# Kernel optimization log

Measured on AMD Instinct MI355X. Metric: run time of the kernel, lower is better.

The kernel has to match this reference:

```python
import jax, jax.numpy as jnp
import numpy as np

B, S, D, H = 2, 2048, 1024, 16
DK = D // H

def setup_inputs() -> dict:
    key = jax.random.key(0)
    ks = jax.random.split(key, 7)
    q = jax.random.normal(ks[0], (B, S, D), dtype=jnp.float32)
    k = jax.random.normal(ks[1], (B, S, D), dtype=jnp.float32)
    v = jax.random.normal(ks[2], (B, S, D), dtype=jnp.float32)
    # causal mask, broadcastable to [B, H, S, S]
    mask = jnp.tril(jnp.ones((S, S), dtype=jnp.int32))[None, None, :, :]
    sc = 1.0 / np.sqrt(D)
    Wq = jax.random.normal(ks[3], (D, D), dtype=jnp.float32) * sc
    Wk = jax.random.normal(ks[4], (D, D), dtype=jnp.float32) * sc
    Wv = jax.random.normal(ks[5], (D, D), dtype=jnp.float32) * sc
    Wo = jax.random.normal(ks[6], (D, D), dtype=jnp.float32) * sc
    return {"q": q, "k": k, "v": v, "mask": mask, "Wq": Wq, "Wk": Wk, "Wv": Wv, "Wo": Wo}

def reference(q, k, v, mask, Wq, Wk, Wv, Wo):
    # Linear projections (nn.Linear stores W as [out,in]; y = x @ W.T; here W is [D,D])
    query = jnp.einsum('bsd,ed->bse', q, Wq).reshape(B, S, H, DK).transpose(0, 2, 1, 3)
    key_  = jnp.einsum('bsd,ed->bse', k, Wk).reshape(B, S, H, DK).transpose(0, 2, 1, 3)
    value = jnp.einsum('bsd,ed->bse', v, Wv).reshape(B, S, H, DK).transpose(0, 2, 1, 3)
    # scaled dot-product attention, full [B,H,S,S] scores (as in the original)
    scaled_qk = jnp.einsum('bhqd,bhkd->bhqk', query, key_) / np.sqrt(DK)
    scaled_qk = jnp.where(mask == 0, jnp.float32(-1e9), scaled_qk)
    scores = jax.nn.softmax(scaled_qk, axis=-1)
    # dropout_rate = 0.0 -> identity
    attn = jnp.einsum('bhqk,bhkd->bhqd', scores, value)
    x = attn.transpose(0, 2, 1, 3).reshape(B, S, D)
    return jnp.einsum('bsd,ed->bse', x, Wo)
```

## Files before the change

### kernel.cpp

```cpp
#include <hip/hip_runtime.h>

constexpr int Bv  = 2;
constexpr int Sv  = 2048;
constexpr int Dv  = 1024;
constexpr int Hv  = 16;
constexpr int DKv = 64;
constexpr int NTOK = Bv * Sv;

#define QSCALE 0.18033688011112042f

typedef __attribute__((ext_vector_type(8))) short bf16x8;
typedef __attribute__((ext_vector_type(4))) float f32x4;

__device__ __forceinline__ ushort f2bf(float f) {
  unsigned int u = __float_as_uint(f);
  unsigned int r = (u + 0x7fffu + ((u >> 16) & 1u)) >> 16;
  return (ushort)r;
}

__device__ __forceinline__ float fast_exp2(float x) {
#if __has_builtin(__builtin_amdgcn_exp2f)
  return __builtin_amdgcn_exp2f(x);
#else
  return exp2f(x);
#endif
}

__device__ __forceinline__ int swz(int byte_linear, int row) {
  return byte_linear ^ ((row & 7) << 4);
}

__device__ __forceinline__ void cast_octet(const float* __restrict__ src,
                                           ushort* __restrict__ dst, int o) {
  const float4 f0 = *reinterpret_cast<const float4*>(src + (size_t)o * 8);
  const float4 f1 = *reinterpret_cast<const float4*>(src + (size_t)o * 8 + 4);
  uint4 u;
  u.x = (unsigned int)f2bf(f0.x) | ((unsigned int)f2bf(f0.y) << 16);
  u.y = (unsigned int)f2bf(f0.z) | ((unsigned int)f2bf(f0.w) << 16);
  u.z = (unsigned int)f2bf(f1.x) | ((unsigned int)f2bf(f1.y) << 16);
  u.w = (unsigned int)f2bf(f1.z) | ((unsigned int)f2bf(f1.w) << 16);
  *reinterpret_cast<uint4*>(dst + (size_t)o * 8) = u;
}

__device__ __forceinline__ void split_octet(const float* __restrict__ src,
                                            ushort* __restrict__ dst, int o) {
  const float4 f0 = *reinterpret_cast<const float4*>(src + (size_t)o * 8);
  const float4 f1 = *reinterpret_cast<const float4*>(src + (size_t)o * 8 + 4);
  float xs[8] = {f0.x, f0.y, f0.z, f0.w, f1.x, f1.y, f1.z, f1.w};
  unsigned int hp[4], lp[4];
#pragma unroll
  for (int j = 0; j < 4; ++j) {
    const unsigned int u0 = __float_as_uint(xs[2 * j]);
    const unsigned int u1 = __float_as_uint(xs[2 * j + 1]);
    const unsigned int h0 = u0 & 0xffff0000u;
    const unsigned int h1 = u1 & 0xffff0000u;
    hp[j] = (h0 >> 16) | h1;
    const float r0 = xs[2 * j] - __uint_as_float(h0);
    const float r1 = xs[2 * j + 1] - __uint_as_float(h1);
    lp[j] = (__float_as_uint(r0) >> 16) | (__float_as_uint(r1) & 0xffff0000u);
  }
  uint4* d = reinterpret_cast<uint4*>(dst + (size_t)o * 16);
  d[0] = make_uint4(hp[0], hp[1], hp[2], hp[3]);
  d[1] = make_uint4(lp[0], lp[1], lp[2], lp[3]);
}

__global__ __launch_bounds__(256)
void cast_split(const float* __restrict__ q, const float* __restrict__ k,
                const float* __restrict__ v, const float* __restrict__ Wq,
                const float* __restrict__ Wk, const float* __restrict__ Wv,
                const float* __restrict__ Wo,
                ushort* __restrict__ qB, ushort* __restrict__ kB,
                ushort* __restrict__ vB, ushort* __restrict__ WqB,
                ushort* __restrict__ WkB, ushort* __restrict__ WvB,
                ushort* __restrict__ WoS) {
  const int o = blockIdx.x * 256 + threadIdx.x;
  constexpr int NA = NTOK * Dv / 8;
  constexpr int NW = Dv * Dv / 8;
  switch (blockIdx.y) {
    case 0: if (o < NA) cast_octet(q, qB, o); break;
    case 1: if (o < NA) cast_octet(k, kB, o); break;
    case 2: if (o < NA) cast_octet(v, vB, o); break;
    case 3: if (o < NW) cast_octet(Wq, WqB, o); break;
    case 4: if (o < NW) cast_octet(Wk, WkB, o); break;
    case 5: if (o < NW) cast_octet(Wv, WvB, o); break;
    default: if (o < NW) split_octet(Wo, WoS, o); break;
  }
}

__global__ __launch_bounds__(256)
void split1(const float* __restrict__ src, ushort* __restrict__ dst) {
  const int o = blockIdx.x * 256 + threadIdx.x;
  if (o < NTOK * Dv / 8) split_octet(src, dst, o);
}

__global__ __launch_bounds__(256, 2)
void gemm_qkv_bf16(const ushort* __restrict__ qB, const ushort* __restrict__ kB,
                   const ushort* __restrict__ vB,
                   const ushort* __restrict__ WqB, const ushort* __restrict__ WkB,
                   const ushort* __restrict__ WvB,
                   ushort* __restrict__ Qw, ushort* __restrict__ Kw,
                   ushort* __restrict__ Vw) {
  const int hid = (int)blockIdx.z * 256 + (int)blockIdx.y * 8 + (int)blockIdx.x;
  const int id  = (hid & 7) * 96 + (hid >> 3);
  const int bn = id & 7;
  const int bm = (id >> 3) & 31;
  const int bz = id >> 8;

  const ushort* Ag;
  const ushort* Wg;
  ushort* Y;
  float scale = 1.0f;
  if (bz == 0)      { Ag = qB; Wg = WqB; Y = Qw; scale = QSCALE; }
  else if (bz == 1) { Ag = kB; Wg = WkB; Y = Kw; }
  else              { Ag = vB; Wg = WvB; Y = Vw; }

  __shared__ __align__(16) ushort AT[128 * 128];
  __shared__ __align__(16) ushort WT[128 * 128];

  const int tid  = threadIdx.x;
  const int lane = tid & 63;
  const int wid  = tid >> 6;
  const int wr = wid >> 1, wc = wid & 1;
  const int c = lane & 15, g = lane >> 4;

  f32x4 acc[4][4];
#pragma unroll
  for (int m = 0; m < 4; ++m)
#pragma unroll
    for (int n = 0; n < 4; ++n) acc[m][n] = (f32x4){0.f, 0.f, 0.f, 0.f};

  const int srow  = tid >> 4;
  const int sslot = tid & 15;
  const size_t aBase = (size_t)(bm * 128 + srow) * 1024 + sslot * 8;
  const size_t wBase = (size_t)(bn * 128 + srow) * 1024 + sslot * 8;
  const int sb = srow * 256 + ((sslot * 16) ^ ((srow & 7) << 4));

  for (int kt = 0; kt < 8; ++kt) {
    __syncthreads();
#pragma unroll
    for (int it = 0; it < 8; ++it)
      *reinterpret_cast<uint4*>((char*)AT + it * 4096 + sb) =
          *reinterpret_cast<const uint4*>(Ag + aBase + (size_t)it * 16384 + kt * 128);
#pragma unroll
    for (int it = 0; it < 8; ++it)
      *reinterpret_cast<uint4*>((char*)WT + it * 4096 + sb) =
          *reinterpret_cast<const uint4*>(Wg + wBase + (size_t)it * 16384 + kt * 128);
    __syncthreads();

#pragma unroll
    for (int kk = 0; kk < 4; ++kk) {
      const int ob = kk * 64 + 16 * g;
      bf16x8 bh[4];
#pragma unroll
      for (int n = 0; n < 4; ++n) {
        const int row = wc * 64 + n * 16 + c;
        bh[n] = *reinterpret_cast<const bf16x8*>((const char*)WT + swz(row * 256 + ob, row));
      }
#pragma unroll
      for (int m = 0; m < 4; ++m) {
        const int row = wr * 64 + m * 16 + c;
        const bf16x8 ah = *reinterpret_cast<const bf16x8*>((const char*)AT + swz(row * 256 + ob, row));
#pragma unroll
        for (int n = 0; n < 4; ++n)
          acc[m][n] = __builtin_amdgcn_mfma_f32_16x16x32_bf16(ah, bh[n], acc[m][n], 0, 0, 0);
      }
    }
  }

#pragma unroll
  for (int m = 0; m < 4; ++m)
#pragma unroll
    for (int n = 0; n < 4; ++n)
#pragma unroll
      for (int r = 0; r < 4; ++r) {
        const int tok = bm * 128 + wr * 64 + m * 16 + 4 * g + r;
        const int e   = bn * 128 + wc * 64 + n * 16 + c;
        const int bb = tok >> 11, ss = tok & (Sv - 1);
        const int hh = e >> 6, dk = e & (DKv - 1);
        Y[(((size_t)bb * Hv + hh) * Sv + ss) * DKv + dk] = f2bf(acc[m][n][r] * scale);
      }
}

__global__ __launch_bounds__(256, 2)
void gemm_out_mfma(const ushort* __restrict__ Ag, const ushort* __restrict__ Wg,
                   float* __restrict__ out) {
  const int hid = (int)blockIdx.y * 8 + (int)blockIdx.x;
  const int id  = (hid & 7) * 32 + (hid >> 3);
  const int bn = id & 7;
  const int bm = id >> 3;

  __shared__ __align__(16) ushort AT[128 * 128];
  __shared__ __align__(16) ushort WT[128 * 128];

  const int tid  = threadIdx.x;
  const int lane = tid & 63;
  const int wid  = tid >> 6;
  const int wr = wid >> 1, wc = wid & 1;
  const int c = lane & 15, g = lane >> 4;

  f32x4 acc[4][4];
#pragma unroll
  for (int m = 0; m < 4; ++m)
#pragma unroll
    for (int n = 0; n < 4; ++n) acc[m][n] = (f32x4){0.f, 0.f, 0.f, 0.f};

  const int srow  = tid >> 4;
  const int sslot = tid & 15;
  const size_t aBase = (size_t)(bm * 128 + srow) * 2048 + sslot * 8;
  const size_t wBase = (size_t)(bn * 128 + srow) * 2048 + sslot * 8;
  const int sb = srow * 256 + ((sslot * 16) ^ ((srow & 7) << 4));

  for (int kt = 0; kt < 16; ++kt) {
    __syncthreads();
#pragma unroll
    for (int it = 0; it < 8; ++it)
      *reinterpret_cast<uint4*>((char*)AT + it * 4096 + sb) =
          *reinterpret_cast<const uint4*>(Ag + aBase + (size_t)it * 32768 + kt * 128);
#pragma unroll
    for (int it = 0; it < 8; ++it)
      *reinterpret_cast<uint4*>((char*)WT + it * 4096 + sb) =
          *reinterpret_cast<const uint4*>(Wg + wBase + (size_t)it * 32768 + kt * 128);
    __syncthreads();

#pragma unroll
    for (int kk = 0; kk < 2; ++kk) {
      const int ob = (kk * 4 + g) * 32;
      bf16x8 bh[4], bl[4];
#pragma unroll
      for (int n = 0; n < 4; ++n) {
        const int row = wc * 64 + n * 16 + c;
        const char* p = (const char*)WT;
        bh[n] = *reinterpret_cast<const bf16x8*>(p + swz(row * 256 + ob, row));
        bl[n] = *reinterpret_cast<const bf16x8*>(p + swz(row * 256 + ob + 16, row));
      }
#pragma unroll
      for (int m = 0; m < 4; ++m) {
        const int row = wr * 64 + m * 16 + c;
        const char* p = (const char*)AT;
        const bf16x8 ah = *reinterpret_cast<const bf16x8*>(p + swz(row * 256 + ob, row));
        const bf16x8 al = *reinterpret_cast<const bf16x8*>(p + swz(row * 256 + ob + 16, row));
#pragma unroll
        for (int n = 0; n < 4; ++n) {
          acc[m][n] = __builtin_amdgcn_mfma_f32_16x16x32_bf16(ah, bh[n], acc[m][n], 0, 0, 0);
          acc[m][n] = __builtin_amdgcn_mfma_f32_16x16x32_bf16(al, bh[n], acc[m][n], 0, 0, 0);
          acc[m][n] = __builtin_amdgcn_mfma_f32_16x16x32_bf16(ah, bl[n], acc[m][n], 0, 0, 0);
        }
      }
    }
  }

#pragma unroll
  for (int m = 0; m < 4; ++m)
#pragma unroll
    for (int n = 0; n < 4; ++n)
#pragma unroll
      for (int r = 0; r < 4; ++r) {
        const int tok = bm * 128 + wr * 64 + m * 16 + 4 * g + r;
        const int e   = bn * 128 + wc * 64 + n * 16 + c;
        out[(size_t)tok * Dv + e] = acc[m][n][r];
      }
}

__global__ __launch_bounds__(256)
void attn_fwd_mfma(const ushort* __restrict__ Q, const ushort* __restrict__ K,
                   const ushort* __restrict__ V, float* __restrict__ X) {
  const int tid  = threadIdx.x;
  const int lane = tid & 63;
  const int w    = tid >> 6;
  const int c    = lane & 15;
  const int g    = lane >> 4;
  const int qt = (int)gridDim.x - 1 - (int)blockIdx.x;
  const int bh = blockIdx.y;
  const int b = bh >> 4, h = bh & (Hv - 1);
  const int qtk = 2 * qt + 1;

  const ushort* Qb = Q + (size_t)bh * Sv * DKv;
  const ushort* Kb = K + (size_t)bh * Sv * DKv;
  const ushort* Vb = V + (size_t)bh * Sv * DKv;

  __shared__ __align__(16) char lds[49152];

#pragma unroll
  for (int l = 0; l < 2; ++l) {
    const int r  = l * 64 + (tid >> 2);
    const int c0 = (tid & 3) << 4;
    const ushort* src = Qb + (size_t)(qt * 128 + r) * DKv + c0;
    uint4 v0 = *reinterpret_cast<const uint4*>(src);
    uint4 v1 = *reinterpret_cast<const uint4*>(src + 8);
    *reinterpret_cast<uint4*>(lds + swz(r * 128 + 2 * c0, r))      = v0;
    *reinterpret_cast<uint4*>(lds + swz(r * 128 + 2 * c0 + 16, r)) = v1;
  }
  __syncthreads();

  bf16x8 qf0[2], qf1[2];
#pragma unroll
  for (int m = 0; m < 2; ++m) {
    const int qr = w * 32 + m * 16 + c;
    qf0[m] = *reinterpret_cast<const bf16x8*>(lds + swz(qr * 128 + 16 * g, qr));
    qf1[m] = *reinterpret_cast<const bf16x8*>(lds + swz(qr * 128 + 64 + 16 * g, qr));
  }

  const int kr_s  = tid >> 2;
  const int kc_s  = (tid & 3) << 4;
  const int vi_s  = tid & 31;
  const int vc_s  = (tid >> 5) << 3;

  uint4 kA, kB, vA, vB;
  {
    const ushort* ks = Kb + (size_t)kr_s * DKv + kc_s;
    kA = *reinterpret_cast<const uint4*>(ks);
    kB = *reinterpret_cast<const uint4*>(ks + 8);
    const ushort* vs = Vb + (size_t)(2 * vi_s) * DKv + vc_s;
    vA = *reinterpret_cast<const uint4*>(vs);
    vB = *reinterpret_cast<const uint4*>(vs + DKv);
  }
  __syncthreads();

  {
    char* kd = lds;
    *reinterpret_cast<uint4*>(kd + swz(kr_s * 128 + 2 * kc_s, kr_s))      = kA;
    *reinterpret_cast<uint4*>(kd + swz(kr_s * 128 + 2 * kc_s + 16, kr_s)) = kB;
    char* vd = lds + 16384;
    unsigned int ee[4] = {vA.x, vA.y, vA.z, vA.w};
    unsigned int oo[4] = {vB.x, vB.y, vB.z, vB.w};
#pragma unroll
    for (int p = 0; p < 4; ++p) {
      unsigned int lo = (ee[p] & 0xffffu) | (oo[p] << 16);
      unsigned int hi = (ee[p] >> 16) | (oo[p] & 0xffff0000u);
      const int d0 = vc_s + 2 * p;
      *reinterpret_cast<unsigned int*>(vd + swz(d0 * 128 + 4 * vi_s, d0))           = lo;
      *reinterpret_cast<unsigned int*>(vd + swz((d0 + 1) * 128 + 4 * vi_s, d0 + 1)) = hi;
    }
  }
  __syncthreads();

  f32x4 accO[2][4];
#pragma unroll
  for (int m = 0; m < 2; ++m)
#pragma unroll
    for (int ds = 0; ds < 4; ++ds) accO[m][ds] = (f32x4){0.f, 0.f, 0.f, 0.f};
  float mS[2] = {-3.0e38f, -3.0e38f};
  float lS[2] = {0.f, 0.f};

  for (int kv = 0; kv <= qtk; ++kv) {
    const int cur = kv & 1;

    if (kv < qtk) {
      const ushort* ks = Kb + (size_t)((kv + 1) * 64 + kr_s) * DKv + kc_s;
      kA = *reinterpret_cast<const uint4*>(ks);
      kB = *reinterpret_cast<const uint4*>(ks + 8);
      const ushort* vs = Vb + (size_t)((kv + 1) * 64 + 2 * vi_s) * DKv + vc_s;
      vA = *reinterpret_cast<const uint4*>(vs);
      vB = *reinterpret_cast<const uint4*>(vs + DKv);
    }

    const char* kbase = lds + cur * 8192;
    const char* vbase = lds + 16384 + cur * 8192;
    char* pbase = lds + 32768 + w * 4096;

    f32x4 s[2][4];
#pragma unroll
    for (int kt = 0; kt < 4; ++kt) {
      const int kr = kt * 16 + c;
      bf16x8 kf0 = *reinterpret_cast<const bf16x8*>(kbase + swz(kr * 128 + 16 * g, kr));
      bf16x8 kf1 = *reinterpret_cast<const bf16x8*>(kbase + swz(kr * 128 + 64 + 16 * g, kr));
#pragma unroll
      for (int m = 0; m < 2; ++m) {
        f32x4 z = (f32x4){0.f, 0.f, 0.f, 0.f};
        z = __builtin_amdgcn_mfma_f32_16x16x32_bf16(kf0, qf0[m], z, 0, 0, 0);
        s[m][kt] = __builtin_amdgcn_mfma_f32_16x16x32_bf16(kf1, qf1[m], z, 0, 0, 0);
      }
    }

    if (kv >= 2 * qt) {
#pragma unroll
      for (int m = 0; m < 2; ++m) {
        const int ql = qt * 128 + w * 32 + m * 16 + c;
#pragma unroll
        for (int kt = 0; kt < 4; ++kt)
#pragma unroll
          for (int rr = 0; rr < 4; ++rr) {
            const int kl = kv * 64 + kt * 16 + 4 * g + rr;
            if (kl > ql) s[m][kt][rr] = -3.0e38f;
          }
      }
    }

    float corrM[2];
#pragma unroll
    for (int m = 0; m < 2; ++m) {
      float tm = -3.0e38f;
#pragma unroll
      for (int kt = 0; kt < 4; ++kt)
#pragma unroll
        for (int rr = 0; rr < 4; ++rr) tm = fmaxf(tm, s[m][kt][rr]);
      tm = fmaxf(tm, __shfl_xor(tm, 16));
      tm = fmaxf(tm, __shfl_xor(tm, 32));
      const float mnew = fmaxf(mS[m], tm);
      corrM[m] = fast_exp2(mS[m] - mnew);
      mS[m] = mnew;

      float psum = 0.f;
#pragma unroll
      for (int kt = 0; kt < 4; ++kt)
#pragma unroll
        for (int rr = 0; rr < 4; ++rr) {
          const float p = fast_exp2(s[m][kt][rr] - mnew);
          s[m][kt][rr] = p;
          psum += p;
        }
      psum += __shfl_xor(psum, 16);
      psum += __shfl_xor(psum, 32);
      lS[m] = lS[m] * corrM[m] + psum;

      const int pr = m * 16 + c;
#pragma unroll
      for (int kt = 0; kt < 4; ++kt) {
        unsigned int lo = (unsigned int)f2bf(s[m][kt][0]) | ((unsigned int)f2bf(s[m][kt][1]) << 16);
        unsigned int hi = (unsigned int)f2bf(s[m][kt][2]) | ((unsigned int)f2bf(s[m][kt][3]) << 16);
        const int k0 = kt * 16 + 4 * g;
        *reinterpret_cast<unsigned int*>(pbase + swz(pr * 128 + 2 * k0, pr))     = lo;
        *reinterpret_cast<unsigned int*>(pbase + swz(pr * 128 + 2 * k0 + 4, pr)) = hi;
      }

      float corr4[4];
#pragma unroll
      for (int rr = 0; rr < 4; ++rr)
        corr4[rr] = __int_as_float(__builtin_amdgcn_ds_bpermute(
            (4 * g + rr) << 2, __float_as_int(corrM[m])));
#pragma unroll
      for (int ds = 0; ds < 4; ++ds)
#pragma unroll
        for (int rr = 0; rr < 4; ++rr) accO[m][ds][rr] *= corr4[rr];
    }

#pragma unroll
    for (int ks = 0; ks < 2; ++ks) {
      bf16x8 vf[4];
#pragma unroll
      for (int ds = 0; ds < 4; ++ds) {
        const int dk = ds * 16 + c;
        vf[ds] = *reinterpret_cast<const bf16x8*>(vbase + swz(dk * 128 + ks * 64 + 16 * g, dk));
      }
#pragma unroll
      for (int m = 0; m < 2; ++m) {
        const int pr = m * 16 + c;
        bf16x8 pf = *reinterpret_cast<const bf16x8*>(pbase + swz(pr * 128 + ks * 64 + 16 * g, pr));
#pragma unroll
        for (int ds = 0; ds < 4; ++ds)
          accO[m][ds] = __builtin_amdgcn_mfma_f32_16x16x32_bf16(pf, vf[ds], accO[m][ds], 0, 0, 0);
      }
    }

    if (kv < qtk) {
      char* kd = lds + (cur ^ 1) * 8192;
      *reinterpret_cast<uint4*>(kd + swz(kr_s * 128 + 2 * kc_s, kr_s))      = kA;
      *reinterpret_cast<uint4*>(kd + swz(kr_s * 128 + 2 * kc_s + 16, kr_s)) = kB;
      char* vd = lds + 16384 + (cur ^ 1) * 8192;
      unsigned int ee[4] = {vA.x, vA.y, vA.z, vA.w};
      unsigned int oo[4] = {vB.x, vB.y, vB.z, vB.w};
#pragma unroll
      for (int p = 0; p < 4; ++p) {
        unsigned int lo = (ee[p] & 0xffffu) | (oo[p] << 16);
        unsigned int hi = (ee[p] >> 16) | (oo[p] & 0xffff0000u);
        const int d0 = vc_s + 2 * p;
        *reinterpret_cast<unsigned int*>(vd + swz(d0 * 128 + 4 * vi_s, d0))           = lo;
        *reinterpret_cast<unsigned int*>(vd + swz((d0 + 1) * 128 + 4 * vi_s, d0 + 1)) = hi;
      }
    }
    __syncthreads();
  }

#pragma unroll
  for (int m = 0; m < 2; ++m) {
    const float inv = 1.0f / lS[m];
    float inv4[4];
#pragma unroll
    for (int rr = 0; rr < 4; ++rr)
      inv4[rr] = __int_as_float(__builtin_amdgcn_ds_bpermute(
          (4 * g + rr) << 2, __float_as_int(inv)));
    const int q0 = qt * 128 + w * 32 + m * 16;
#pragma unroll
    for (int ds = 0; ds < 4; ++ds)
#pragma unroll
      for (int rr = 0; rr < 4; ++rr) {
        const int srow = q0 + 4 * g + rr;
        X[((size_t)(b * Sv + srow)) * Dv + h * DKv + ds * 16 + c] = accO[m][ds][rr] * inv4[rr];
      }
  }
}

extern "C" void kernel_launch(void* const* d_in, const int* in_sizes, int n_in,
                              void* d_out, int out_size, void* d_ws, size_t ws_size,
                              hipStream_t stream) {
  const float* q  = (const float*)d_in[0];
  const float* k  = (const float*)d_in[1];
  const float* v  = (const float*)d_in[2];
  const float* Wq = (const float*)d_in[4];
  const float* Wk = (const float*)d_in[5];
  const float* Wv = (const float*)d_in[6];
  const float* Wo = (const float*)d_in[7];
  float* out = (float*)d_out;

  constexpr size_t SEG   = (size_t)NTOK * Dv;
  constexpr size_t ACT_S = SEG * 2;
  constexpr size_t X_S   = SEG * 4;
  constexpr size_t WB_S  = (size_t)Dv * Dv * 2;
  constexpr size_t SPW_S = (size_t)Dv * Dv * 4;

  char* ws = (char*)d_ws;
  ushort* Qw  = (ushort*)(ws);
  ushort* Kw  = (ushort*)(ws + ACT_S);
  ushort* Vw  = (ushort*)(ws + 2 * ACT_S);
  float*  Xw  = (float*) (ws + 3 * ACT_S);
  ushort* qB  = (ushort*)(ws + 3 * ACT_S + X_S);
  ushort* kB  = (ushort*)(ws + 3 * ACT_S + X_S + ACT_S);
  ushort* vB  = (ushort*)(ws + 3 * ACT_S + X_S + 2 * ACT_S);
  ushort* WqB = (ushort*)(ws + 3 * ACT_S + X_S + 3 * ACT_S);
  ushort* WkB = (ushort*)(ws + 3 * ACT_S + X_S + 3 * ACT_S + WB_S);
  ushort* WvB = (ushort*)(ws + 3 * ACT_S + X_S + 3 * ACT_S + 2 * WB_S);
  ushort* WoS = (ushort*)(ws + 3 * ACT_S + X_S + 3 * ACT_S + 3 * WB_S);
  ushort* XS  = (ushort*)(ws + 3 * ACT_S + X_S + 3 * ACT_S + 3 * WB_S + SPW_S);

  const dim3 blk(256);
  cast_split<<<dim3(NTOK * Dv / 8 / 256, 7), blk, 0, stream>>>(
      q, k, v, Wq, Wk, Wv, Wo, qB, kB, vB, WqB, WkB, WvB, WoS);
  gemm_qkv_bf16<<<dim3(8, 32, 3), blk, 0, stream>>>(
      qB, kB, vB, WqB, WkB, WvB, Qw, Kw, Vw);
  attn_fwd_mfma<<<dim3(Sv / 128, Bv * Hv), blk, 0, stream>>>(Qw, Kw, Vw, Xw);
  split1<<<dim3(NTOK * Dv / 8 / 256), blk, 0, stream>>>(Xw, XS);
  gemm_out_mfma<<<dim3(8, 32), blk, 0, stream>>>(XS, WoS, out);
}
```

Measured before the change: 275.5 us.

## Fuse bf16 hi/lo split into attention epilogue and balance causal work per block

```diff
diff --git a/kernel.cpp b/kernel.cpp
--- a/kernel.cpp
+++ b/kernel.cpp
@@ -87,12 +87,6 @@
   }
 }
 
-__global__ __launch_bounds__(256)
-void split1(const float* __restrict__ src, ushort* __restrict__ dst) {
-  const int o = blockIdx.x * 256 + threadIdx.x;
-  if (o < NTOK * Dv / 8) split_octet(src, dst, o);
-}
-
 __global__ __launch_bounds__(256, 2)
 void gemm_qkv_bf16(const ushort* __restrict__ qB, const ushort* __restrict__ kB,
                    const ushort* __restrict__ vB,
@@ -261,202 +255,65 @@
       }
 }
 
-__global__ __launch_bounds__(256)
+__global__ __launch_bounds__(512)
 void attn_fwd_mfma(const ushort* __restrict__ Q, const ushort* __restrict__ K,
-                   const ushort* __restrict__ V, float* __restrict__ X) {
+                   const ushort* __restrict__ V, ushort* __restrict__ XS) {
   const int tid  = threadIdx.x;
   const int lane = tid & 63;
   const int w    = tid >> 6;
   const int c    = lane & 15;
   const int g    = lane >> 4;
-  const int qt = (int)gridDim.x - 1 - (int)blockIdx.x;
-  const int bh = blockIdx.y;
-  const int b = bh >> 4, h = bh & (Hv - 1);
-  const int qtk = 2 * qt + 1;
-
-  const ushort* Qb = Q + (size_t)bh * Sv * DKv;
-  const ushort* Kb = K + (size_t)bh * Sv * DKv;
-  const ushort* Vb = V + (size_t)bh * Sv * DKv;
 
   __shared__ __align__(16) char lds[49152];
 
-#pragma unroll
-  for (int l = 0; l < 2; ++l) {
-    const int r  = l * 64 + (tid >> 2);
-    const int c0 = (tid & 3) << 4;
-    const ushort* src = Qb + (size_t)(qt * 128 + r) * DKv + c0;
-    uint4 v0 = *reinterpret_cast<const uint4*>(src);
-    uint4 v1 = *reinterpret_cast<const uint4*>(src + 8);
-    *reinterpret_cast<uint4*>(lds + swz(r * 128 + 2 * c0, r))      = v0;
-    *reinterpret_cast<uint4*>(lds + swz(r * 128 + 2 * c0 + 16, r)) = v1;
-  }
-  __syncthreads();
-
-  bf16x8 qf0[2], qf1[2];
-#pragma unroll
-  for (int m = 0; m < 2; ++m) {
-    const int qr = w * 32 + m * 16 + c;
-    qf0[m] = *reinterpret_cast<const bf16x8*>(lds + swz(qr * 128 + 16 * g, qr));
-    qf1[m] = *reinterpret_cast<const bf16x8*>(lds + swz(qr * 128 + 64 + 16 * g, qr));
-  }
-
-  const int kr_s  = tid >> 2;
-  const int kc_s  = (tid & 3) << 4;
-  const int vi_s  = tid & 31;
-  const int vc_s  = (tid >> 5) << 3;
-
-  uint4 kA, kB, vA, vB;
-  {
-    const ushort* ks = Kb + (size_t)kr_s * DKv + kc_s;
-    kA = *reinterpret_cast<const uint4*>(ks);
-    kB = *reinterpret_cast<const uint4*>(ks + 8);
-    const ushort* vs = Vb + (size_t)(2 * vi_s) * DKv + vc_s;
-    vA = *reinterpret_cast<const uint4*>(vs);
-    vB = *reinterpret_cast<const uint4*>(vs + DKv);
-  }
-  __syncthreads();
-
-  {
-    char* kd = lds;
-    *reinterpret_cast<uint4*>(kd + swz(kr_s * 128 + 2 * kc_s, kr_s))      = kA;
-    *reinterpret_cast<uint4*>(kd + swz(kr_s * 128 + 2 * kc_s + 16, kr_s)) = kB;
-    char* vd = lds + 16384;
-    unsigned int ee[4] = {vA.x, vA.y, vA.z, vA.w};
-    unsigned int oo[4] = {vB.x, vB.y, vB.z, vB.w};
-#pragma unroll
-    for (int p = 0; p < 4; ++p) {
-      unsigned int lo = (ee[p] & 0xffffu) | (oo[p] << 16);
-      unsigned int hi = (ee[p] >> 16) | (oo[p] & 0xffff0000u);
-      const int d0 = vc_s + 2 * p;
-      *reinterpret_cast<unsigned int*>(vd + swz(d0 * 128 + 4 * vi_s, d0))           = lo;
-      *reinterpret_cast<unsigned int*>(vd + swz((d0 + 1) * 128 + 4 * vi_s, d0 + 1)) = hi;
-    }
-  }
-  __syncthreads();
-
-  f32x4 accO[2][4];
-#pragma unroll
-  for (int m = 0; m < 2; ++m)
-#pragma unroll
-    for (int ds = 0; ds < 4; ++ds) accO[m][ds] = (f32x4){0.f, 0.f, 0.f, 0.f};
-  float mS[2] = {-3.0e38f, -3.0e38f};
-  float lS[2] = {0.f, 0.f};
-
-  for (int kv = 0; kv <= qtk; ++kv) {
-    const int cur = kv & 1;
-
-    if (kv < qtk) {
-      const ushort* ks = Kb + (size_t)((kv + 1) * 64 + kr_s) * DKv + kc_s;
-      kA = *reinterpret_cast<const uint4*>(ks);
-      kB = *reinterpret_cast<const uint4*>(ks + 8);
-      const ushort* vs = Vb + (size_t)((kv + 1) * 64 + 2 * vi_s) * DKv + vc_s;
+  const int kr_s = tid >> 3;
+  const int kcb  = (tid & 7) << 4;
+  const bool vwork = (tid < 256);
+  const int vi_s = tid & 31;
+  const int vc_s = ((tid >> 5) & 7) << 3;
+
+#pragma unroll 1
+  for (int item = 0; item < 2; ++item) {
+    const int idx = (item == 0) ? (int)blockIdx.x : 511 - (int)blockIdx.x;
+    const int qt = idx >> 5;
+    const int bh = idx & 31;
+    const int b = bh >> 4, h = bh & (Hv - 1);
+    const int qtk = 2 * qt + 1;
+
+    const ushort* Qb = Q + (size_t)bh * Sv * DKv;
+    const ushort* Kb = K + (size_t)bh * Sv * DKv;
+    const ushort* Vb = V + (size_t)bh * Sv * DKv;
+
+    {
+      const int r  = tid >> 2;
+      const int c0 = (tid & 3) << 4;
+      const ushort* src = Qb + (size_t)(qt * 128 + r) * DKv + c0;
+      uint4 v0 = *reinterpret_cast<const uint4*>(src);
+      uint4 v1 = *reinterpret_cast<const uint4*>(src + 8);
+      *reinterpret_cast<uint4*>(lds + swz(r * 128 + 2 * c0, r))      = v0;
+      *reinterpret_cast<uint4*>(lds + swz(r * 128 + 2 * c0 + 16, r)) = v1;
+    }
+    __syncthreads();
+
+    bf16x8 qf0, qf1;
+    {
+      const int qr = w * 16 + c;
+      qf0 = *reinterpret_cast<const bf16x8*>(lds + swz(qr * 128 + 16 * g, qr));
+      qf1 = *reinterpret_cast<const bf16x8*>(lds + swz(qr * 128 + 64 + 16 * g, qr));
+    }
+
+    uint4 kA, vA, vB;
+    kA = *reinterpret_cast<const uint4*>((const char*)Kb + (size_t)kr_s * 128 + kcb);
+    if (vwork) {
+      const ushort* vs = Vb + (size_t)(2 * vi_s) * DKv + vc_s;
       vA = *reinterpret_cast<const uint4*>(vs);
       vB = *reinterpret_cast<const uint4*>(vs + DKv);
     }
-
-    const char* kbase = lds + cur * 8192;
-    const char* vbase = lds + 16384 + cur * 8192;
-    char* pbase = lds + 32768 + w * 4096;
-
-    f32x4 s[2][4];
-#pragma unroll
-    for (int kt = 0; kt < 4; ++kt) {
-      const int kr = kt * 16 + c;
-      bf16x8 kf0 = *reinterpret_cast<const bf16x8*>(kbase + swz(kr * 128 + 16 * g, kr));
-      bf16x8 kf1 = *reinterpret_cast<const bf16x8*>(kbase + swz(kr * 128 + 64 + 16 * g, kr));
-#pragma unroll
-      for (int m = 0; m < 2; ++m) {
-        f32x4 z = (f32x4){0.f, 0.f, 0.f, 0.f};
-        z = __builtin_amdgcn_mfma_f32_16x16x32_bf16(kf0, qf0[m], z, 0, 0, 0);
-        s[m][kt] = __builtin_amdgcn_mfma_f32_16x16x32_bf16(kf1, qf1[m], z, 0, 0, 0);
-      }
-    }
-
-    if (kv >= 2 * qt) {
-#pragma unroll
-      for (int m = 0; m < 2; ++m) {
-        const int ql = qt * 128 + w * 32 + m * 16 + c;
-#pragma unroll
-        for (int kt = 0; kt < 4; ++kt)
-#pragma unroll
-          for (int rr = 0; rr < 4; ++rr) {
-            const int kl = kv * 64 + kt * 16 + 4 * g + rr;
-            if (kl > ql) s[m][kt][rr] = -3.0e38f;
-          }
-      }
-    }
-
-    float corrM[2];
-#pragma unroll
-    for (int m = 0; m < 2; ++m) {
-      float tm = -3.0e38f;
-#pragma unroll
-      for (int kt = 0; kt < 4; ++kt)
-#pragma unroll
-        for (int rr = 0; rr < 4; ++rr) tm = fmaxf(tm, s[m][kt][rr]);
-      tm = fmaxf(tm, __shfl_xor(tm, 16));
-      tm = fmaxf(tm, __shfl_xor(tm, 32));
-      const float mnew = fmaxf(mS[m], tm);
-      corrM[m] = fast_exp2(mS[m] - mnew);
-      mS[m] = mnew;
-
-      float psum = 0.f;
-#pragma unroll
-      for (int kt = 0; kt < 4; ++kt)
-#pragma unroll
-        for (int rr = 0; rr < 4; ++rr) {
-          const float p = fast_exp2(s[m][kt][rr] - mnew);
-          s[m][kt][rr] = p;
-          psum += p;
-        }
-      psum += __shfl_xor(psum, 16);
-      psum += __shfl_xor(psum, 32);
-      lS[m] = lS[m] * corrM[m] + psum;
-
-      const int pr = m * 16 + c;
-#pragma unroll
-      for (int kt = 0; kt < 4; ++kt) {
-        unsigned int lo = (unsigned int)f2bf(s[m][kt][0]) | ((unsigned int)f2bf(s[m][kt][1]) << 16);
-        unsigned int hi = (unsigned int)f2bf(s[m][kt][2]) | ((unsigned int)f2bf(s[m][kt][3]) << 16);
-        const int k0 = kt * 16 + 4 * g;
-        *reinterpret_cast<unsigned int*>(pbase + swz(pr * 128 + 2 * k0, pr))     = lo;
-        *reinterpret_cast<unsigned int*>(pbase + swz(pr * 128 + 2 * k0 + 4, pr)) = hi;
-      }
-
-      float corr4[4];
-#pragma unroll
-      for (int rr = 0; rr < 4; ++rr)
-        corr4[rr] = __int_as_float(__builtin_amdgcn_ds_bpermute(
-            (4 * g + rr) << 2, __float_as_int(corrM[m])));
-#pragma unroll
-      for (int ds = 0; ds < 4; ++ds)
-#pragma unroll
-        for (int rr = 0; rr < 4; ++rr) accO[m][ds][rr] *= corr4[rr];
-    }
-
-#pragma unroll
-    for (int ks = 0; ks < 2; ++ks) {
-      bf16x8 vf[4];
-#pragma unroll
-      for (int ds = 0; ds < 4; ++ds) {
-        const int dk = ds * 16 + c;
-        vf[ds] = *reinterpret_cast<const bf16x8*>(vbase + swz(dk * 128 + ks * 64 + 16 * g, dk));
-      }
-#pragma unroll
-      for (int m = 0; m < 2; ++m) {
-        const int pr = m * 16 + c;
-        bf16x8 pf = *reinterpret_cast<const bf16x8*>(pbase + swz(pr * 128 + ks * 64 + 16 * g, pr));
-#pragma unroll
-        for (int ds = 0; ds < 4; ++ds)
-          accO[m][ds] = __builtin_amdgcn_mfma_f32_16x16x32_bf16(pf, vf[ds], accO[m][ds], 0, 0, 0);
-      }
-    }
-
-    if (kv < qtk) {
-      char* kd = lds + (cur ^ 1) * 8192;
-      *reinterpret_cast<uint4*>(kd + swz(kr_s * 128 + 2 * kc_s, kr_s))      = kA;
-      *reinterpret_cast<uint4*>(kd + swz(kr_s * 128 + 2 * kc_s + 16, kr_s)) = kB;
-      char* vd = lds + 16384 + (cur ^ 1) * 8192;
+    __syncthreads();
+
+    *reinterpret_cast<uint4*>(lds + swz(kr_s * 128 + kcb, kr_s)) = kA;
+    if (vwork) {
+      char* vd = lds + 16384;
       unsigned int ee[4] = {vA.x, vA.y, vA.z, vA.w};
       unsigned int oo[4] = {vB.x, vB.y, vB.z, vB.w};
 #pragma unroll
@@ -469,24 +326,151 @@
       }
     }
     __syncthreads();
-  }
-
-#pragma unroll
-  for (int m = 0; m < 2; ++m) {
-    const float inv = 1.0f / lS[m];
-    float inv4[4];
-#pragma unroll
-    for (int rr = 0; rr < 4; ++rr)
-      inv4[rr] = __int_as_float(__builtin_amdgcn_ds_bpermute(
-          (4 * g + rr) << 2, __float_as_int(inv)));
-    const int q0 = qt * 128 + w * 32 + m * 16;
-#pragma unroll
-    for (int ds = 0; ds < 4; ++ds)
-#pragma unroll
-      for (int rr = 0; rr < 4; ++rr) {
-        const int srow = q0 + 4 * g + rr;
-        X[((size_t)(b * Sv + srow)) * Dv + h * DKv + ds * 16 + c] = accO[m][ds][rr] * inv4[rr];
-      }
+
+    f32x4 accO[4];
+#pragma unroll
+    for (int ds = 0; ds < 4; ++ds) accO[ds] = (f32x4){0.f, 0.f, 0.f, 0.f};
+    float mS = -3.0e38f, lS = 0.f;
+
+    for (int kv = 0; kv <= qtk; ++kv) {
+      const int cur = kv & 1;
+
+      if (kv < qtk) {
+        kA = *reinterpret_cast<const uint4*>(
+            (const char*)Kb + ((size_t)(kv + 1) * 64 + kr_s) * 128 + kcb);
+        if (vwork) {
+          const ushort* vs = Vb + (size_t)((kv + 1) * 64 + 2 * vi_s) * DKv + vc_s;
+          vA = *reinterpret_cast<const uint4*>(vs);
+          vB = *reinterpret_cast<const uint4*>(vs + DKv);
+        }
+      }
+
+      const char* kbase = lds + cur * 8192;
+      const char* vbase = lds + 16384 + cur * 8192;
+      char* pbase = lds + 32768 + w * 2048;
+
+      f32x4 s[4];
+#pragma unroll
+      for (int kt = 0; kt < 4; ++kt) {
+        const int kr = kt * 16 + c;
+        bf16x8 kf0 = *reinterpret_cast<const bf16x8*>(kbase + swz(kr * 128 + 16 * g, kr));
+        bf16x8 kf1 = *reinterpret_cast<const bf16x8*>(kbase + swz(kr * 128 + 64 + 16 * g, kr));
+        f32x4 z = (f32x4){0.f, 0.f, 0.f, 0.f};
+        z = __builtin_amdgcn_mfma_f32_16x16x32_bf16(kf0, qf0, z, 0, 0, 0);
+        s[kt] = __builtin_amdgcn_mfma_f32_16x16x32_bf16(kf1, qf1, z, 0, 0, 0);
+      }
+
+      if (kv >= 2 * qt) {
+        const int ql = qt * 128 + w * 16 + c;
+#pragma unroll
+        for (int kt = 0; kt < 4; ++kt)
+#pragma unroll
+          for (int rr = 0; rr < 4; ++rr) {
+            const int kl = kv * 64 + kt * 16 + 4 * g + rr;
+            if (kl > ql) s[kt][rr] = -3.0e38f;
+          }
+      }
+
+      float tm = -3.0e38f;
+#pragma unroll
+      for (int kt = 0; kt < 4; ++kt)
+#pragma unroll
+        for (int rr = 0; rr < 4; ++rr) tm = fmaxf(tm, s[kt][rr]);
+      tm = fmaxf(tm, __shfl_xor(tm, 16));
+      tm = fmaxf(tm, __shfl_xor(tm, 32));
+      const float mnew = fmaxf(mS, tm);
+      const float corr = fast_exp2(mS - mnew);
+      mS = mnew;
+
+      float psum = 0.f;
+#pragma unroll
+      for (int kt = 0; kt < 4; ++kt)
+#pragma unroll
+        for (int rr = 0; rr < 4; ++rr) {
+          const float p = fast_exp2(s[kt][rr] - mnew);
+          s[kt][rr] = p;
+          psum += p;
+        }
+      psum += __shfl_xor(psum, 16);
+      psum += __shfl_xor(psum, 32);
+      lS = lS * corr + psum;
+
+#pragma unroll
+      for (int kt = 0; kt < 4; ++kt) {
+        unsigned int lo = (unsigned int)f2bf(s[kt][0]) | ((unsigned int)f2bf(s[kt][1]) << 16);
+        unsigned int hi = (unsigned int)f2bf(s[kt][2]) | ((unsigned int)f2bf(s[kt][3]) << 16);
+        const int k0 = kt * 16 + 4 * g;
+        *reinterpret_cast<unsigned int*>(pbase + swz(c * 128 + 2 * k0, c))     = lo;
+        *reinterpret_cast<unsigned int*>(pbase + swz(c * 128 + 2 * k0 + 4, c)) = hi;
+      }
+
+      float corr4[4];
+#pragma unroll
+      for (int rr = 0; rr < 4; ++rr)
+        corr4[rr] = __int_as_float(__builtin_amdgcn_ds_bpermute(
+            (4 * g + rr) << 2, __float_as_int(corr)));
+#pragma unroll
+      for (int ds = 0; ds < 4; ++ds)
+#pragma unroll
+        for (int rr = 0; rr < 4; ++rr) accO[ds][rr] *= corr4[rr];
+
+#pragma unroll
+      for (int ks = 0; ks < 2; ++ks) {
+        bf16x8 pf = *reinterpret_cast<const bf16x8*>(pbase + swz(c * 128 + ks * 64 + 16 * g, c));
+#pragma unroll
+        for (int ds = 0; ds < 4; ++ds) {
+          const int dk = ds * 16 + c;
+          bf16x8 vf = *reinterpret_cast<const bf16x8*>(vbase + swz(dk * 128 + ks * 64 + 16 * g, dk));
+          accO[ds] = __builtin_amdgcn_mfma_f32_16x16x32_bf16(pf, vf, accO[ds], 0, 0, 0);
+        }
+      }
+
+      if (kv < qtk) {
+        char* kd = lds + (cur ^ 1) * 8192;
+        *reinterpret_cast<uint4*>(kd + swz(kr_s * 128 + kcb, kr_s)) = kA;
+        if (vwork) {
+          char* vd = lds + 16384 + (cur ^ 1) * 8192;
+          unsigned int ee[4] = {vA.x, vA.y, vA.z, vA.w};
+          unsigned int oo[4] = {vB.x, vB.y, vB.z, vB.w};
+#pragma unroll
+          for (int p = 0; p < 4; ++p) {
+            unsigned int lo = (ee[p] & 0xffffu) | (oo[p] << 16);
+            unsigned int hi = (ee[p] >> 16) | (oo[p] & 0xffff0000u);
+            const int d0 = vc_s + 2 * p;
+            *reinterpret_cast<unsigned int*>(vd + swz(d0 * 128 + 4 * vi_s, d0))           = lo;
+            *reinterpret_cast<unsigned int*>(vd + swz((d0 + 1) * 128 + 4 * vi_s, d0 + 1)) = hi;
+          }
+        }
+      }
+      __syncthreads();
+    }
+
+    {
+      const float inv = 1.0f / lS;
+      float inv4[4];
+#pragma unroll
+      for (int rr = 0; rr < 4; ++rr)
+        inv4[rr] = __int_as_float(__builtin_amdgcn_ds_bpermute(
+            (4 * g + rr) << 2, __float_as_int(inv)));
+      const int q0 = qt * 128 + w * 16;
+#pragma unroll
+      for (int ds = 0; ds < 4; ++ds) {
+        const int e   = h * DKv + ds * 16 + c;
+        const int oct = e >> 3, j = e & 7;
+#pragma unroll
+        for (int rr = 0; rr < 4; ++rr) {
+          const int srow = q0 + 4 * g + rr;
+          const float y = accO[ds][rr] * inv4[rr];
+          const unsigned int u  = __float_as_uint(y);
+          const unsigned int hb = u & 0xffff0000u;
+          const float rlo = y - __uint_as_float(hb);
+          ushort* d = XS + ((size_t)(b * Sv + srow)) * 2048 + oct * 16 + j;
+          d[0] = (ushort)(u >> 16);
+          d[8] = (ushort)(__float_as_uint(rlo) >> 16);
+        }
+      }
+    }
+    if (item == 0) __syncthreads();
   }
 }
 
@@ -512,7 +496,6 @@
   ushort* Qw  = (ushort*)(ws);
   ushort* Kw  = (ushort*)(ws + ACT_S);
   ushort* Vw  = (ushort*)(ws + 2 * ACT_S);
-  float*  Xw  = (float*) (ws + 3 * ACT_S);
   ushort* qB  = (ushort*)(ws + 3 * ACT_S + X_S);
   ushort* kB  = (ushort*)(ws + 3 * ACT_S + X_S + ACT_S);
   ushort* vB  = (ushort*)(ws + 3 * ACT_S + X_S + 2 * ACT_S);
@@ -527,7 +510,6 @@
       q, k, v, Wq, Wk, Wv, Wo, qB, kB, vB, WqB, WkB, WvB, WoS);
   gemm_qkv_bf16<<<dim3(8, 32, 3), blk, 0, stream>>>(
       qB, kB, vB, WqB, WkB, WvB, Qw, Kw, Vw);
-  attn_fwd_mfma<<<dim3(Sv / 128, Bv * Hv), blk, 0, stream>>>(Qw, Kw, Vw, Xw);
-  split1<<<dim3(NTOK * Dv / 8 / 256), blk, 0, stream>>>(Xw, XS);
+  attn_fwd_mfma<<<dim3(256), dim3(512), 0, stream>>>(Qw, Kw, Vw, XS);
   gemm_out_mfma<<<dim3(8, 32), blk, 0, stream>>>(XS, WoS, out);
 }
```

New measurement: 239.2 us. 13.2% less time.
